# Kernel optimization log

Hardware: AMD Instinct MI355X
Metric: run time of the kernel (lower is better)

The kernel has to match this reference:

```python
import jax, jax.numpy as jnp
import numpy as np

B, T = 4, 1024
V = 1024          # vocab_size (tied to block_size via weight tying)
BLK = 1024        # block_size
C = 768           # n_embd
H = 12            # n_head
HS = C // H       # head_size = 64
L = 6             # n_layer
F = 4 * C         # FFN hidden
STD = 0.02
EPS = 1e-5


def layer_norm(x, w, b):
    m = x.mean(-1, keepdims=True)
    v = ((x - m) ** 2).mean(-1, keepdims=True)
    return (x - m) / jnp.sqrt(v + EPS) * w + b


def setup_inputs() -> dict:
    key = jax.random.key(0)
    ks = jax.random.split(key, 12)
    n = lambda k, shape: jax.random.normal(k, shape, dtype=jnp.float32) * STD
    inp = {
        "idx": jax.random.randint(ks[0], (B, T), 0, V),
        "targets": jax.random.randint(ks[1], (B, T), 0, V),
        "wte": n(ks[2], (V, C)),            # tied with lm_head weight
        "wpe": n(ks[3], (BLK, C)),
        "lm_b": jnp.zeros((V,), jnp.float32),
        "ln1_w": jnp.ones((L, C), jnp.float32),
        "ln1_b": jnp.zeros((L, C), jnp.float32),
        "Wq": n(ks[4], (L, C, C)),           # per-layer stacked head projections (head-major columns)
        "Wk": n(ks[5], (L, C, C)),
        "Wv": n(ks[6], (L, C, C)),
        "proj_W": n(ks[7], (L, C, C)),
        "proj_b": jnp.zeros((L, C), jnp.float32),
        "ln2_w": jnp.ones((L, C), jnp.float32),
        "ln2_b": jnp.zeros((L, C), jnp.float32),
        "fc1_W": n(ks[8], (L, C, F)),
        "fc1_b": jnp.zeros((L, F), jnp.float32),
        "fc2_W": n(ks[9], (L, F, C)),
        "fc2_b": jnp.zeros((L, C), jnp.float32),
        "lnf_w": jnp.ones((C,), jnp.float32),
        "lnf_b": jnp.zeros((C,), jnp.float32),
    }
    return inp


def reference(idx, targets, wte, wpe, lm_b, ln1_w, ln1_b, Wq, Wk, Wv,
              proj_W, proj_b, ln2_w, ln2_b, fc1_W, fc1_b, fc2_W, fc2_b,
              lnf_w, lnf_b):
    Bc, Tc = idx.shape
    x = wte[idx] + wpe[jnp.arange(Tc)]          # [B,T,C]
    mask = jnp.tril(jnp.ones((Tc, Tc), bool))   # causal tril buffer
    neg_inf = jnp.asarray(-jnp.inf, x.dtype)
    for l in range(L):
        h = layer_norm(x, ln1_w[l], ln1_b[l])
        q = (h @ Wq[l]).reshape(Bc, Tc, H, HS)
        k = (h @ Wk[l]).reshape(Bc, Tc, H, HS)
        v = (h @ Wv[l]).reshape(Bc, Tc, H, HS)
        wei = jnp.einsum('bqhd,bkhd->bhqk', q, k) * (HS ** -0.5)
        wei = jnp.where(mask, wei, neg_inf)
        wei = jax.nn.softmax(wei, axis=-1)
        att = jnp.einsum('bhqk,bkhd->bqhd', wei, v).reshape(Bc, Tc, C)
        x = att @ proj_W[l] + proj_b[l] + x
        h2 = layer_norm(x, ln2_w[l], ln2_b[l])
        x = jax.nn.relu(h2 @ fc1_W[l] + fc1_b[l]) @ fc2_W[l] + fc2_b[l] + x
    x = layer_norm(x, lnf_w, lnf_b)
    logits = x @ wte.T + lm_b                   # weight-tied lm_head
    logp = jax.nn.log_softmax(logits, axis=-1)
    loss = -jnp.take_along_axis(logp, targets[..., None], axis=-1).mean()
    return logits, loss
```

## Files before the change

### kernel.cpp

```cpp
#include <hip/hip_runtime.h>
#include <hip/hip_bf16.h>

typedef short bf16x8 __attribute__((ext_vector_type(8)));
typedef unsigned short u16x8 __attribute__((ext_vector_type(8)));
typedef float f32x4 __attribute__((ext_vector_type(4)));

#define B_ 4
#define T_ 1024
#define V_ 1024
#define C_ 768
#define H_ 12
#define HS_ 64
#define L_ 6
#define F_ 3072
#define M_ (B_ * T_)
#define QKV_ 2304

__device__ inline float b2f(unsigned short u) {
    return __uint_as_float(((unsigned int)u) << 16);
}
__device__ inline unsigned short f2bbits(float f) {
    __hip_bfloat16 h = __float2bfloat16(f);
    return *(unsigned short*)&h;
}
__device__ inline void load_lds_16(const void* g, void* l) {
    __builtin_amdgcn_global_load_lds(
        (const __attribute__((address_space(1))) unsigned int*)g,
        (__attribute__((address_space(3))) unsigned int*)l, 16, 0, 0);
}

__global__ void convert_bf16_kernel(const float* __restrict__ in,
                                    __hip_bfloat16* __restrict__ out, int n) {
    int i = blockIdx.x * 256 + threadIdx.x;
    if (i < n) out[i] = __float2bfloat16(in[i]);
}

__global__ void embed_kernel(const int* __restrict__ idx,
                             const float* __restrict__ wte,
                             const float* __restrict__ wpe,
                             float* __restrict__ x) {
    int i = blockIdx.x * 256 + threadIdx.x;
    int row = i / C_;
    int c = i - row * C_;
    int t = row & (T_ - 1);
    x[i] = wte[(size_t)idx[row] * C_ + c] + wpe[(size_t)t * C_ + c];
}

__global__ __launch_bounds__(256) void ln4_kernel(const float* __restrict__ x,
                                                  const float* __restrict__ w,
                                                  const float* __restrict__ b,
                                                  __hip_bfloat16* __restrict__ out) {
    int row = blockIdx.x * 4 + (threadIdx.x >> 6);
    int lane = threadIdx.x & 63;
    const float* xr = x + (size_t)row * C_;
    float v[12];
    float s = 0.0f;
    #pragma unroll
    for (int j = 0; j < 12; j++) { v[j] = xr[lane + 64 * j]; s += v[j]; }
    #pragma unroll
    for (int o = 32; o; o >>= 1) s += __shfl_xor(s, o);
    float mean = s * (1.0f / C_);
    float vs = 0.0f;
    #pragma unroll
    for (int j = 0; j < 12; j++) { v[j] -= mean; vs += v[j] * v[j]; }
    #pragma unroll
    for (int o = 32; o; o >>= 1) vs += __shfl_xor(vs, o);
    float rstd = rsqrtf(vs * (1.0f / C_) + 1e-5f);
    __hip_bfloat16* o = out + (size_t)row * C_;
    #pragma unroll
    for (int j = 0; j < 12; j++) {
        int c = lane + 64 * j;
        o[c] = __float2bfloat16(v[j] * rstd * w[c] + b[c]);
    }
}

__global__ void transpose_bf16_kernel(const float* __restrict__ W,
                                      __hip_bfloat16* __restrict__ WT,
                                      int K, int N,
                                      size_t sStride, size_t dStride) {
    int l = blockIdx.z;
    W += (size_t)l * sStride;
    WT += (size_t)l * dStride;
    __shared__ float tile[32][33];
    int n0 = blockIdx.x * 32, k0 = blockIdx.y * 32;
    int tx = threadIdx.x, ty = threadIdx.y;
    #pragma unroll
    for (int i = 0; i < 4; i++)
        tile[ty + 8 * i][tx] = W[(size_t)(k0 + ty + 8 * i) * N + n0 + tx];
    __syncthreads();
    #pragma unroll
    for (int i = 0; i < 4; i++)
        WT[(size_t)(n0 + ty + 8 * i) * K + k0 + tx] =
            __float2bfloat16(tile[tx][ty + 8 * i]);
}

__global__ void transpose_qkv_kernel(const float* __restrict__ Wq,
                                     const float* __restrict__ Wk,
                                     const float* __restrict__ Wv,
                                     __hip_bfloat16* __restrict__ dst) {
    int z = blockIdx.z;
    int l = z / 3, which = z % 3;
    const float* W = (which == 0 ? Wq : which == 1 ? Wk : Wv) + (size_t)l * C_ * C_;
    __hip_bfloat16* WT = dst + (size_t)l * QKV_ * C_ + (size_t)which * C_ * C_;
    __shared__ float tile[32][33];
    int n0 = blockIdx.x * 32, k0 = blockIdx.y * 32;
    int tx = threadIdx.x, ty = threadIdx.y;
    #pragma unroll
    for (int i = 0; i < 4; i++)
        tile[ty + 8 * i][tx] = W[(size_t)(k0 + ty + 8 * i) * C_ + n0 + tx];
    __syncthreads();
    #pragma unroll
    for (int i = 0; i < 4; i++)
        WT[(size_t)(n0 + ty + 8 * i) * C_ + k0 + tx] =
            __float2bfloat16(tile[tx][ty + 8 * i]);
}

template <int BN, bool BIAS, bool RES, bool RELU, bool OUTF, bool OUTB>
__global__ __launch_bounds__(256) void gemm64xN_kernel(
    const __hip_bfloat16* __restrict__ A,
    const __hip_bfloat16* __restrict__ WT,
    const float* __restrict__ bias,
    const float* __restrict__ res,
    float* __restrict__ outF,
    __hip_bfloat16* __restrict__ outB,
    int M, int N, int K, int nbx) {
    constexpr int BJ = BN / 32;
    __shared__ __align__(16) short As[2 * 64 * 64];
    __shared__ __align__(16) short Bs[2 * BN * 64];
    int tid = threadIdx.x;
    int lane = tid & 63;
    int w = tid >> 6;
    int l15 = lane & 15, l4 = lane >> 4;

    int nwg = gridDim.x;
    int bid = blockIdx.x;
    int sbid = (bid & 7) * (nwg >> 3) + (bid >> 3);
    int bx = sbid % nbx, by = sbid / nbx;
    int row0 = by * 64, col0 = bx * BN;

    int wr = w >> 1, wc = w & 1;

    int rr = tid >> 3;
    int cswz = (((tid & 7) ^ (rr & 7)) * 8);
    const char* Ag = (const char*)A + ((size_t)(row0 + rr) * K + cswz) * 2;
    const char* Bg = (const char*)WT + ((size_t)(col0 + rr) * K + cswz) * 2;

    f32x4 acc[2][BJ] = {};
    int ktiles = K >> 6;

    auto stage = [&](int buf, int k0) {
        const char* Agk = Ag + (size_t)k0 * 2;
        const char* Bgk = Bg + (size_t)k0 * 2;
        #pragma unroll
        for (int i = 0; i < 2; i++)
            load_lds_16(Agk + (size_t)i * 32 * K * 2,
                        (char*)As + buf * 8192 + i * 4096 + w * 1024);
        #pragma unroll
        for (int i = 0; i < BN / 32; i++)
            load_lds_16(Bgk + (size_t)i * 32 * K * 2,
                        (char*)Bs + buf * (BN * 128) + i * 4096 + w * 1024);
    };

    stage(0, 0);
    int cur = 0;
    int rxor = (l15 & 7) << 4;
    for (int t = 0; t < ktiles; ++t) {
        if (t + 1 < ktiles) {
            stage(cur ^ 1, (t + 1) * 64);
            if constexpr (BN == 128)
                asm volatile("s_waitcnt vmcnt(6)" ::: "memory");
            else
                asm volatile("s_waitcnt vmcnt(4)" ::: "memory");
        } else {
            asm volatile("s_waitcnt vmcnt(0)" ::: "memory");
        }
        __builtin_amdgcn_s_barrier();
        asm volatile("" ::: "memory");
        const char* Asb = (const char*)As + cur * 8192;
        const char* Bsb = (const char*)Bs + cur * (BN * 128);
        #pragma unroll
        for (int kk = 0; kk < 2; kk++) {
            bf16x8 a[2], b[BJ];
            #pragma unroll
            for (int i = 0; i < 2; i++)
                a[i] = *(const bf16x8*)(Asb +
                        (wr * 32 + i * 16 + l15) * 128 + ((kk * 64 + l4 * 16) ^ rxor));
            #pragma unroll
            for (int j = 0; j < BJ; j++)
                b[j] = *(const bf16x8*)(Bsb +
                        (wc * (BN / 2) + j * 16 + l15) * 128 + ((kk * 64 + l4 * 16) ^ rxor));
            #pragma unroll
            for (int i = 0; i < 2; i++)
                #pragma unroll
                for (int j = 0; j < BJ; j++)
                    acc[i][j] = __builtin_amdgcn_mfma_f32_16x16x32_bf16(
                        a[i], b[j], acc[i][j], 0, 0, 0);
        }
        asm volatile("" ::: "memory");
        __builtin_amdgcn_s_barrier();
        cur ^= 1;
    }

    int rbase = l4 * 4;
    #pragma unroll
    for (int i = 0; i < 2; i++) {
        #pragma unroll
        for (int j = 0; j < BJ; j++) {
            int col = col0 + wc * (BN / 2) + j * 16 + l15;
            float bv = BIAS ? bias[col] : 0.0f;
            #pragma unroll
            for (int r = 0; r < 4; r++) {
                int row = row0 + wr * 32 + i * 16 + rbase + r;
                size_t off = (size_t)row * N + col;
                float v = acc[i][j][r] + bv;
                if (RES) v += res[off];
                if (RELU) v = fmaxf(v, 0.0f);
                if (OUTF) outF[off] = v;
                if (OUTB) outB[off] = __float2bfloat16(v);
            }
        }
    }
}

__global__ __launch_bounds__(512) void attn_flash_kernel(
    const __hip_bfloat16* __restrict__ qkvb,
    __hip_bfloat16* __restrict__ attb) {
    int tid = threadIdx.x;
    int lane = tid & 63;
    int w = tid >> 6;
    int l15 = lane & 15;
    int l4 = lane >> 4;

    int bid = blockIdx.x;
    int xcd = bid & 7, i = bid >> 3;
    int qc = 7 - (i / 6);
    int bh = (i % 6) * 8 + xcd;
    int b = bh / H_, h = bh % H_;
    int qb0 = qc * 128;

    __shared__ __align__(16) unsigned short Ks[64 * 64];
    __shared__ __align__(16) unsigned short Vt[64 * 64];
    __shared__ __align__(16) unsigned short Ps[8 * 16 * 64];

    const unsigned short* qkv = (const unsigned short*)qkvb;
    const unsigned short* Qg = qkv + (size_t)(b * T_ + qb0) * QKV_ + h * HS_;
    const unsigned short* Kg = qkv + (size_t)b * T_ * QKV_ + C_ + h * HS_;
    const unsigned short* Vg = qkv + (size_t)b * T_ * QKV_ + 2 * C_ + h * HS_;

    bf16x8 qfrag[2];
    {
        const short* qrow = (const short*)Qg + (size_t)(w * 16 + l15) * QKV_;
        qfrag[0] = *(const bf16x8*)(qrow + l4 * 8);
        qfrag[1] = *(const bf16x8*)(qrow + 32 + l4 * 8);
    }

    f32x4 o_acc[4] = {};
    float m_run[4], l_run[4];
    #pragma unroll
    for (int r = 0; r < 4; r++) { m_run[r] = -1e30f; l_run[r] = 0.0f; }

    unsigned short* Pw = Ps + w * 16 * 64;
    int nkb = (qc + 1) * 2;

    for (int kbi = 0; kbi < nkb; ++kbi) {
        int k0 = kbi * 64;
        __syncthreads();
        {
            int key = tid >> 3, ch = tid & 7;
            u16x8 kv = *(const u16x8*)(Kg + (size_t)(k0 + key) * QKV_ + ch * 8);
            int byteoff = key * 128 + ((ch * 16) ^ ((key & 7) << 4));
            *(u16x8*)((char*)Ks + byteoff) = kv;

            u16x8 vv = *(const u16x8*)(Vg + (size_t)(k0 + key) * QKV_ + ch * 8);
            #pragma unroll
            for (int e = 0; e < 8; ++e) {
                int d = ch * 8 + e;
                int slot = (d ^ (d >> 3)) & 7;
                int boff = d * 128 + ((key * 2) ^ (slot << 4));
                *(unsigned short*)((char*)Vt + boff) = (unsigned short)vv[e];
            }
        }
        __syncthreads();

        f32x4 s[4] = {};
        #pragma unroll
        for (int kk = 0; kk < 2; ++kk) {
            #pragma unroll
            for (int nt = 0; nt < 4; ++nt) {
                int key = nt * 16 + l15;
                int boff = key * 128 + (((l4 * 16) + kk * 64) ^ ((key & 7) << 4));
                bf16x8 kf = *(const bf16x8*)((char*)Ks + boff);
                s[nt] = __builtin_amdgcn_mfma_f32_16x16x32_bf16(qfrag[kk], kf, s[nt], 0, 0, 0);
            }
        }

        bool maskt = (kbi >= 2 * qc);
        #pragma unroll
        for (int nt = 0; nt < 4; ++nt)
            #pragma unroll
            for (int r = 0; r < 4; ++r) {
                float v = s[nt][r] * 0.125f;
                if (maskt) {
                    int key = k0 + nt * 16 + l15;
                    int q = qb0 + w * 16 + l4 * 4 + r;
                    if (key > q) v = -1e30f;
                }
                s[nt][r] = v;
            }

        #pragma unroll
        for (int r = 0; r < 4; ++r) {
            float mx = fmaxf(fmaxf(s[0][r], s[1][r]), fmaxf(s[2][r], s[3][r]));
            #pragma unroll
            for (int o = 8; o; o >>= 1) mx = fmaxf(mx, __shfl_xor(mx, o));
            float mnew = fmaxf(m_run[r], mx);
            float alpha = __expf(m_run[r] - mnew);
            m_run[r] = mnew;
            float rs = 0.0f;
            #pragma unroll
            for (int nt = 0; nt < 4; ++nt) {
                float p = __expf(s[nt][r] - mnew);
                s[nt][r] = p;
                rs += p;
            }
            #pragma unroll
            for (int o = 8; o; o >>= 1) rs += __shfl_xor(rs, o);
            l_run[r] = l_run[r] * alpha + rs;
            #pragma unroll
            for (int nt = 0; nt < 4; ++nt) o_acc[nt][r] *= alpha;
        }

        #pragma unroll
        for (int nt = 0; nt < 4; ++nt)
            #pragma unroll
            for (int r = 0; r < 4; ++r) {
                int q = l4 * 4 + r;
                int col = nt * 16 + l15;
                int boff = q * 128 + ((col * 2) ^ ((q & 7) << 4));
                *(unsigned short*)((char*)Pw + boff) = f2bbits(s[nt][r]);
            }

        #pragma unroll
        for (int kk = 0; kk < 2; ++kk) {
            int q = l15;
            int pboff = q * 128 + (((l4 * 16) + kk * 64) ^ ((q & 7) << 4));
            bf16x8 pf = *(const bf16x8*)((char*)Pw + pboff);
            #pragma unroll
            for (int nt = 0; nt < 4; ++nt) {
                int d = nt * 16 + l15;
                int dslot = (d ^ (d >> 3)) & 7;
                int vboff = d * 128 + (((l4 * 16) + kk * 64) ^ (dslot << 4));
                bf16x8 vf = *(const bf16x8*)((char*)Vt + vboff);
                o_acc[nt] = __builtin_amdgcn_mfma_f32_16x16x32_bf16(pf, vf, o_acc[nt], 0, 0, 0);
            }
        }
    }

    unsigned short* Og = (unsigned short*)attb + (size_t)(b * T_ + qb0) * C_ + h * HS_;
    #pragma unroll
    for (int r = 0; r < 4; ++r) {
        float inv = 1.0f / l_run[r];
        #pragma unroll
        for (int nt = 0; nt < 4; ++nt) {
            float val = o_acc[nt][r] * inv;
            Og[(size_t)(w * 16 + l4 * 4 + r) * C_ + nt * 16 + l15] = f2bbits(val);
        }
    }
}

__global__ void loss_rows_kernel(const float* __restrict__ logits,
                                 const int* __restrict__ targets,
                                 float* __restrict__ partials) {
    int row = blockIdx.x, tid = threadIdx.x;
    const float* lr = logits + (size_t)row * V_;
    __shared__ float red[256];
    float mx = -1e30f;
    for (int i = tid; i < V_; i += 256) mx = fmaxf(mx, lr[i]);
    red[tid] = mx;
    __syncthreads();
    for (int s = 128; s; s >>= 1) {
        if (tid < s) red[tid] = fmaxf(red[tid], red[tid + s]);
        __syncthreads();
    }
    mx = red[0];
    __syncthreads();
    float sum = 0.0f;
    for (int i = tid; i < V_; i += 256) sum += __expf(lr[i] - mx);
    red[tid] = sum;
    __syncthreads();
    for (int s = 128; s; s >>= 1) {
        if (tid < s) red[tid] += red[tid + s];
        __syncthreads();
    }
    if (tid == 0) {
        float lse = mx + __logf(red[0]);
        partials[row] = lse - lr[targets[row]];
    }
}

__global__ void loss_reduce_kernel(const float* __restrict__ partials,
                                   float* __restrict__ out) {
    int tid = threadIdx.x;
    float s = 0.0f;
    for (int i = tid; i < M_; i += 256) s += partials[i];
    __shared__ float red[256];
    red[tid] = s;
    __syncthreads();
    for (int st = 128; st; st >>= 1) {
        if (tid < st) red[tid] += red[tid + st];
        __syncthreads();
    }
    if (tid == 0) out[0] = red[0] * (1.0f / M_);
}

extern "C" void kernel_launch(void* const* d_in, const int* in_sizes, int n_in,
                              void* d_out, int out_size, void* d_ws, size_t ws_size,
                              hipStream_t stream) {
    const int*   idx     = (const int*)d_in[0];
    const int*   targets = (const int*)d_in[1];
    const float* wte     = (const float*)d_in[2];
    const float* wpe     = (const float*)d_in[3];
    const float* lm_b    = (const float*)d_in[4];
    const float* ln1_w   = (const float*)d_in[5];
    const float* ln1_b   = (const float*)d_in[6];
    const float* Wq      = (const float*)d_in[7];
    const float* Wk      = (const float*)d_in[8];
    const float* Wv      = (const float*)d_in[9];
    const float* projW   = (const float*)d_in[10];
    const float* projb   = (const float*)d_in[11];
    const float* ln2_w   = (const float*)d_in[12];
    const float* ln2_b   = (const float*)d_in[13];
    const float* fc1W    = (const float*)d_in[14];
    const float* fc1b    = (const float*)d_in[15];
    const float* fc2W    = (const float*)d_in[16];
    const float* fc2b    = (const float*)d_in[17];
    const float* lnfw    = (const float*)d_in[18];
    const float* lnfb    = (const float*)d_in[19];

    char* ws = (char*)d_ws;
    size_t off = 0;
    float* x = (float*)(ws + off);                 off += (size_t)M_ * C_ * 4;
    __hip_bfloat16* h    = (__hip_bfloat16*)(ws + off); off += (size_t)M_ * C_ * 2;
    size_t qkv_off = off;
    __hip_bfloat16* qkvb = (__hip_bfloat16*)(ws + off); off += (size_t)M_ * QKV_ * 2;
    __hip_bfloat16* attb = (__hip_bfloat16*)(ws + off); off += (size_t)M_ * C_ * 2;
    __hip_bfloat16* fb   = (__hip_bfloat16*)(ws + qkv_off);
    __hip_bfloat16* wteB = (__hip_bfloat16*)(ws + off); off += (size_t)V_ * C_ * 2;
    float* partials = (float*)(ws + off);          off += (size_t)M_ * 4;

    const size_t QKV_SZ = (size_t)QKV_ * C_;
    const size_t WP_SZ  = (size_t)C_ * C_;
    const size_t F1_SZ  = (size_t)C_ * F_;
    const size_t F2_SZ  = (size_t)F_ * C_;
    size_t upfront_bytes = off + 2 * (size_t)L_ * (QKV_SZ + WP_SZ + F1_SZ + F2_SZ);
    bool upfront = ws_size >= upfront_bytes;
    int rep = upfront ? L_ : 1;

    __hip_bfloat16* qkvT0 = (__hip_bfloat16*)(ws + off); off += 2 * (size_t)rep * QKV_SZ;
    __hip_bfloat16* wpT0  = (__hip_bfloat16*)(ws + off); off += 2 * (size_t)rep * WP_SZ;
    __hip_bfloat16* wf1T0 = (__hip_bfloat16*)(ws + off); off += 2 * (size_t)rep * F1_SZ;
    __hip_bfloat16* wf2T0 = (__hip_bfloat16*)(ws + off); off += 2 * (size_t)rep * F2_SZ;

    float* logits = (float*)d_out;
    float* loss   = (float*)d_out + (size_t)M_ * V_;

    convert_bf16_kernel<<<(V_ * C_ + 255) / 256, 256, 0, stream>>>(wte, wteB, V_ * C_);
    embed_kernel<<<(M_ * C_) / 256, 256, 0, stream>>>(idx, wte, wpe, x);

    if (upfront) {
        transpose_qkv_kernel<<<dim3(C_ / 32, C_ / 32, 3 * L_), dim3(32, 8), 0, stream>>>(
            Wq, Wk, Wv, qkvT0);
        transpose_bf16_kernel<<<dim3(C_ / 32, C_ / 32, L_), dim3(32, 8), 0, stream>>>(
            projW, wpT0, C_, C_, WP_SZ, WP_SZ);
        transpose_bf16_kernel<<<dim3(F_ / 32, C_ / 32, L_), dim3(32, 8), 0, stream>>>(
            fc1W, wf1T0, C_, F_, F1_SZ, F1_SZ);
        transpose_bf16_kernel<<<dim3(C_ / 32, F_ / 32, L_), dim3(32, 8), 0, stream>>>(
            fc2W, wf2T0, F_, C_, F2_SZ, F2_SZ);
    }

    for (int l = 0; l < L_; l++) {
        __hip_bfloat16* qkvT = qkvT0 + (upfront ? (size_t)l * QKV_SZ : 0);
        __hip_bfloat16* wpT  = wpT0  + (upfront ? (size_t)l * WP_SZ : 0);
        __hip_bfloat16* wf1T = wf1T0 + (upfront ? (size_t)l * F1_SZ : 0);
        __hip_bfloat16* wf2T = wf2T0 + (upfront ? (size_t)l * F2_SZ : 0);

        ln4_kernel<<<M_ / 4, 256, 0, stream>>>(x, ln1_w + l * C_, ln1_b + l * C_, h);

        if (!upfront)
            transpose_qkv_kernel<<<dim3(C_ / 32, C_ / 32, 3), dim3(32, 8), 0, stream>>>(
                Wq + (size_t)l * C_ * C_, Wk + (size_t)l * C_ * C_,
                Wv + (size_t)l * C_ * C_, qkvT);

        gemm64xN_kernel<128, false, false, false, false, true>
            <<<(M_ / 64) * (QKV_ / 128), 256, 0, stream>>>(
            h, qkvT, nullptr, nullptr, nullptr, qkvb, M_, QKV_, C_, QKV_ / 128);

        attn_flash_kernel<<<B_ * H_ * (T_ / 128), 512, 0, stream>>>(qkvb, attb);

        if (!upfront)
            transpose_bf16_kernel<<<dim3(C_ / 32, C_ / 32, 1), dim3(32, 8), 0, stream>>>(
                projW + (size_t)l * C_ * C_, wpT, C_, C_, 0, 0);
        gemm64xN_kernel<64, true, true, false, true, false>
            <<<(M_ / 64) * (C_ / 64), 256, 0, stream>>>(
            attb, wpT, projb + l * C_, x, x, nullptr, M_, C_, C_, C_ / 64);

        ln4_kernel<<<M_ / 4, 256, 0, stream>>>(x, ln2_w + l * C_, ln2_b + l * C_, h);

        if (!upfront)
            transpose_bf16_kernel<<<dim3(F_ / 32, C_ / 32, 1), dim3(32, 8), 0, stream>>>(
                fc1W + (size_t)l * C_ * F_, wf1T, C_, F_, 0, 0);
        gemm64xN_kernel<128, true, false, true, false, true>
            <<<(M_ / 64) * (F_ / 128), 256, 0, stream>>>(
            h, wf1T, fc1b + l * F_, nullptr, nullptr, fb, M_, F_, C_, F_ / 128);

        if (!upfront)
            transpose_bf16_kernel<<<dim3(C_ / 32, F_ / 32, 1), dim3(32, 8), 0, stream>>>(
                fc2W + (size_t)l * F_ * C_, wf2T, F_, C_, 0, 0);
        gemm64xN_kernel<64, true, true, false, true, false>
            <<<(M_ / 64) * (C_ / 64), 256, 0, stream>>>(
            fb, wf2T, fc2b + l * C_, x, x, nullptr, M_, C_, F_, C_ / 64);
    }

    ln4_kernel<<<M_ / 4, 256, 0, stream>>>(x, lnfw, lnfb, h);
    gemm64xN_kernel<128, true, false, false, true, false>
        <<<(M_ / 64) * (V_ / 128), 256, 0, stream>>>(
        h, wteB, lm_b, nullptr, logits, nullptr, M_, V_, C_, V_ / 128);

    loss_rows_kernel<<<M_, 256, 0, stream>>>(logits, targets, partials);
    loss_reduce_kernel<<<1, 256, 0, stream>>>(partials, loss);
}
```

Before: 1.024 ms.

## Double-buffer K/V tiles in flash attention with register prefetch and MFMA priority

```diff
diff --git a/kernel.cpp b/kernel.cpp
--- a/kernel.cpp
+++ b/kernel.cpp
@@ -238,8 +238,8 @@
     int b = bh / H_, h = bh % H_;
     int qb0 = qc * 128;
 
-    __shared__ __align__(16) unsigned short Ks[64 * 64];
-    __shared__ __align__(16) unsigned short Vt[64 * 64];
+    __shared__ __align__(16) unsigned short Ks[2][64 * 64];
+    __shared__ __align__(16) unsigned short Vt[2][64 * 64];
     __shared__ __align__(16) unsigned short Ps[8 * 16 * 64];
 
     const unsigned short* qkv = (const unsigned short*)qkvb;
@@ -262,37 +262,43 @@
     unsigned short* Pw = Ps + w * 16 * 64;
     int nkb = (qc + 1) * 2;
 
+    int key = tid >> 3, ch = tid & 7;
+    int kbyte = key * 128 + ((ch * 16) ^ ((key & 7) << 4));
+
+    u16x8 kreg = *(const u16x8*)(Kg + (size_t)key * QKV_ + ch * 8);
+    u16x8 vreg = *(const u16x8*)(Vg + (size_t)key * QKV_ + ch * 8);
+    *(u16x8*)((char*)Ks[0] + kbyte) = kreg;
+    #pragma unroll
+    for (int e = 0; e < 8; ++e) {
+        int d = ch * 8 + e;
+        int slot = (d ^ (d >> 3)) & 7;
+        *(unsigned short*)((char*)Vt[0] + d * 128 + ((key * 2) ^ (slot << 4))) =
+            (unsigned short)vreg[e];
+    }
+
+    int cur = 0;
     for (int kbi = 0; kbi < nkb; ++kbi) {
         int k0 = kbi * 64;
         __syncthreads();
-        {
-            int key = tid >> 3, ch = tid & 7;
-            u16x8 kv = *(const u16x8*)(Kg + (size_t)(k0 + key) * QKV_ + ch * 8);
-            int byteoff = key * 128 + ((ch * 16) ^ ((key & 7) << 4));
-            *(u16x8*)((char*)Ks + byteoff) = kv;
-
-            u16x8 vv = *(const u16x8*)(Vg + (size_t)(k0 + key) * QKV_ + ch * 8);
-            #pragma unroll
-            for (int e = 0; e < 8; ++e) {
-                int d = ch * 8 + e;
-                int slot = (d ^ (d >> 3)) & 7;
-                int boff = d * 128 + ((key * 2) ^ (slot << 4));
-                *(unsigned short*)((char*)Vt + boff) = (unsigned short)vv[e];
-            }
-        }
-        __syncthreads();
+        bool pref = (kbi + 1 < nkb);
+        if (pref) {
+            kreg = *(const u16x8*)(Kg + (size_t)(k0 + 64 + key) * QKV_ + ch * 8);
+            vreg = *(const u16x8*)(Vg + (size_t)(k0 + 64 + key) * QKV_ + ch * 8);
+        }
 
         f32x4 s[4] = {};
+        __builtin_amdgcn_s_setprio(1);
         #pragma unroll
         for (int kk = 0; kk < 2; ++kk) {
             #pragma unroll
             for (int nt = 0; nt < 4; ++nt) {
-                int key = nt * 16 + l15;
-                int boff = key * 128 + (((l4 * 16) + kk * 64) ^ ((key & 7) << 4));
-                bf16x8 kf = *(const bf16x8*)((char*)Ks + boff);
+                int ky = nt * 16 + l15;
+                int boff = ky * 128 + (((l4 * 16) + kk * 64) ^ ((ky & 7) << 4));
+                bf16x8 kf = *(const bf16x8*)((char*)Ks[cur] + boff);
                 s[nt] = __builtin_amdgcn_mfma_f32_16x16x32_bf16(qfrag[kk], kf, s[nt], 0, 0, 0);
             }
         }
+        __builtin_amdgcn_s_setprio(0);
 
         bool maskt = (kbi >= 2 * qc);
         #pragma unroll
@@ -301,9 +307,9 @@
             for (int r = 0; r < 4; ++r) {
                 float v = s[nt][r] * 0.125f;
                 if (maskt) {
-                    int key = k0 + nt * 16 + l15;
+                    int ky = k0 + nt * 16 + l15;
                     int q = qb0 + w * 16 + l4 * 4 + r;
-                    if (key > q) v = -1e30f;
+                    if (ky > q) v = -1e30f;
                 }
                 s[nt][r] = v;
             }
@@ -340,6 +346,7 @@
                 *(unsigned short*)((char*)Pw + boff) = f2bbits(s[nt][r]);
             }
 
+        __builtin_amdgcn_s_setprio(1);
         #pragma unroll
         for (int kk = 0; kk < 2; ++kk) {
             int q = l15;
@@ -350,10 +357,23 @@
                 int d = nt * 16 + l15;
                 int dslot = (d ^ (d >> 3)) & 7;
                 int vboff = d * 128 + (((l4 * 16) + kk * 64) ^ (dslot << 4));
-                bf16x8 vf = *(const bf16x8*)((char*)Vt + vboff);
+                bf16x8 vf = *(const bf16x8*)((char*)Vt[cur] + vboff);
                 o_acc[nt] = __builtin_amdgcn_mfma_f32_16x16x32_bf16(pf, vf, o_acc[nt], 0, 0, 0);
             }
         }
+        __builtin_amdgcn_s_setprio(0);
+
+        if (pref) {
+            *(u16x8*)((char*)Ks[cur ^ 1] + kbyte) = kreg;
+            #pragma unroll
+            for (int e = 0; e < 8; ++e) {
+                int d = ch * 8 + e;
+                int slot = (d ^ (d >> 3)) & 7;
+                *(unsigned short*)((char*)Vt[cur ^ 1] + d * 128 + ((key * 2) ^ (slot << 4))) =
+                    (unsigned short)vreg[e];
+            }
+        }
+        cur ^= 1;
     }
 
     unsigned short* Og = (unsigned short*)attb + (size_t)(b * T_ + qb0) * C_ + h * HS_;
```

Measured after the change: 1.022 ms. About the same (-0.1%).
